# Kernel tuning notes

Hardware: AMD Instinct MI355X
Metric: run time of the kernel (lower is better)

## Reference

```python
import jax, jax.numpy as jnp
import numpy as np

H = 7      # n_hazards
B = 8      # batch
S = 2048   # seq_len
D = 768    # hidden_dim
K = 64     # bottleneck_dim
THR = 0.05 # influence_threshold


def setup_inputs() -> dict:
    key = jax.random.key(0)
    k0, k1, k2, k3 = jax.random.split(key, 4)
    x = jax.random.normal(k0, (H, B, S, D), jnp.float32)          # stacked hazard reprs
    M = jax.random.normal(k1, (H, H), jnp.float32) * 0.3           # interaction_matrix [src, tgt]
    W1 = jax.random.normal(k2, (H, H, D, K), jnp.float32) * (1.0 / np.sqrt(D).astype(np.float32))
    b1 = jnp.zeros((H, H, K), jnp.float32)
    W2 = jax.random.normal(k3, (H, H, K, D), jnp.float32) * (1.0 / np.sqrt(K).astype(np.float32))
    b2 = jnp.zeros((H, H, D), jnp.float32)
    return {"x": x, "M": M, "W1": W1, "b1": b1, "W2": W2, "b2": b2}


def reference(x, M, W1, b1, W2, b2):
    # Gate: influence used only if |M[s,t]| > threshold and s != t (torch skips the
    # projection entirely below threshold; masking to 0 yields identical values/grads).
    eye = jnp.eye(H, dtype=bool)
    gate = jnp.where((jnp.abs(M) > THR) & (~eye), M, jnp.zeros_like(M))  # [s, t]

    # Bottleneck MLP for all (source, target) pairs in one batched GEMM.
    # h: [s, t, b, n, k]
    h = jnp.einsum('sbnd,stdk->stbnk', x, W1) + b1[:, :, None, None, :]
    h = jax.nn.gelu(h, approximate=False)  # torch nn.GELU default is exact (erf)

    # Fold the scalar gate into the second GEMM so the [s,t,b,n,D] tensor is never
    # materialized; sum over sources lands directly at each target.
    add = jnp.einsum('st,stbnk,stkd->tbnd', gate, h, W2)
    add = add + jnp.einsum('st,std->td', gate, b2)[:, None, None, :]
    return x + add  # [H, B, S, D] stacked in hazard order
```

## Files before the change

kernel.cpp:

```cpp
#include <hip/hip_runtime.h>
#include <hip/hip_bf16.h>
#include <math.h>

#define NH   7
#define NROW 16384
#define DD   768
#define KK   64
#define THRG 0.05f

typedef float  f32x4   __attribute__((ext_vector_type(4)));
typedef __bf16 bf16x8  __attribute__((ext_vector_type(8)));
typedef short  short8v __attribute__((ext_vector_type(8)));
typedef short  short4v __attribute__((ext_vector_type(4)));

union V8 { short8v s; bf16x8 b; };

__device__ __forceinline__ float gate_of(const float* __restrict__ M, int s, int t) {
  float m = M[s * NH + t];
  return (s != t && fabsf(m) > THRG) ? m : 0.0f;
}

__device__ __forceinline__ float gelu_t(float v) {
  float u = 0.7978845608028654f * (v + 0.044715f * v * v * v);
  return v / (1.0f + __expf(-2.0f * u));
}

__device__ __forceinline__ void gload_lds16(const void* g, void* l) {
  __builtin_amdgcn_global_load_lds(
      (const __attribute__((address_space(1))) unsigned int*)g,
      (__attribute__((address_space(3))) unsigned int*)l, 16, 0, 0);
}

__global__ void prep_w1(const float* __restrict__ W1, unsigned short* __restrict__ W1P) {
  int pr = blockIdx.x;
  const float* src = W1 + (size_t)pr * DD * KK;
  __bf16* dst = (__bf16*)(W1P + (size_t)pr * 12 * 4096);
  for (int idx = threadIdx.x; idx < 12 * 4096; idx += blockDim.x) {
    int kc = idx >> 12, rem = idx & 4095;
    int kcol = rem >> 6, dl = rem & 63;
    int dl_log = dl ^ ((kcol & 7) << 3);
    dst[idx] = (__bf16)src[(size_t)(kc * 64 + dl_log) * KK + kcol];
  }
}

__global__ void prep_w2(const float* __restrict__ M, const float* __restrict__ W2,
                        unsigned short* __restrict__ W2P) {
  int st = blockIdx.x;
  int s = st / NH, t = st % NH;
  float g = gate_of(M, s, t);
  const float* src = W2 + (size_t)st * KK * DD;
  __bf16* dst = (__bf16*)(W2P + (size_t)((t * NH + s) * 6) * 8192);
  for (int idx = threadIdx.x; idx < 6 * 128 * 64; idx += blockDim.x) {
    int nb = idx >> 13, rem = idx & 8191;
    int dloc = rem >> 6, k = rem & 63;
    dst[idx] = (__bf16)(g * src[(size_t)k * DD + nb * 128 + dloc]);
  }
}

__global__ void prep_b2(const float* __restrict__ M, const float* __restrict__ b2,
                        float* __restrict__ b2sum) {
  int idx = blockIdx.x * blockDim.x + threadIdx.x;
  if (idx >= NH * DD) return;
  int t = idx / DD, d = idx % DD;
  float acc = 0.f;
  for (int s = 0; s < NH; ++s)
    acc += gate_of(M, s, t) * b2[(size_t)(s * NH + t) * DD + d];
  b2sum[idx] = acc;
}

__global__ __launch_bounds__(256, 3)
void chiA(const float* __restrict__ x, const float* __restrict__ M,
          const unsigned short* __restrict__ W1P, const float* __restrict__ b1,
          unsigned short* __restrict__ H) {
  __shared__ __align__(16) unsigned short xs[128 * 64];
  __shared__ __align__(16) unsigned short w1s[64 * 64];

  int bid = (int)blockIdx.x;
  int nid = (bid & 7) * 784 + (bid >> 3);
  int rb = nid / 49, pr = nid % 49;
  int s = pr / NH, t = pr % NH;
  if (gate_of(M, s, t) == 0.0f) return;
  int row0 = rb * 128;

  int tid = (int)threadIdx.x;
  int wid = tid >> 6, lane = tid & 63, l16 = lane & 15, l4 = lane >> 4;

  const f32x4 zero = {0.f, 0.f, 0.f, 0.f};
  f32x4 acc[4][2];
#pragma unroll
  for (int m = 0; m < 4; ++m)
#pragma unroll
    for (int n = 0; n < 2; ++n) acc[m][n] = zero;

  const float* xb = x + ((size_t)s * NROW + row0) * DD;
  const char* w1b = (const char*)(W1P + (size_t)pr * 12 * 4096);

  for (int kc = 0; kc < 12; ++kc) {
    __syncthreads();
    {
      const char* wsrc = w1b + (size_t)kc * 8192;
      char* wdst = (char*)w1s + (wid << 10);
#pragma unroll
      for (int r = 0; r < 2; ++r)
        gload_lds16(wsrc + r * 4096 + tid * 16, wdst + r * 4096);
    }
#pragma unroll
    for (int r = 0; r < 4; ++r) {
      int L = r * 4096 + tid * 16;
      int row = L >> 7, colB = L & 127;
      const float* gp = xb + (size_t)row * DD + kc * 64 + (colB >> 1);
      f32x4 v0 = *(const f32x4*)gp;
      f32x4 v1 = *(const f32x4*)(gp + 4);
      bf16x8 sv;
      sv[0] = (__bf16)v0[0]; sv[1] = (__bf16)v0[1];
      sv[2] = (__bf16)v0[2]; sv[3] = (__bf16)v0[3];
      sv[4] = (__bf16)v1[0]; sv[5] = (__bf16)v1[1];
      sv[6] = (__bf16)v1[2]; sv[7] = (__bf16)v1[3];
      *(bf16x8*)((char*)xs + (L ^ ((row & 7) << 4))) = sv;
    }
    __syncthreads();

    V8 af[4][2], bf2[2][2];
#pragma unroll
    for (int mm = 0; mm < 4; ++mm)
#pragma unroll
      for (int k2 = 0; k2 < 2; ++k2) {
        int rowl = mm * 16 + l16;
        int byte = (rowl * 128 + k2 * 64 + l4 * 16) ^ ((rowl & 7) << 4);
        af[mm][k2].s = *(const short8v*)((const char*)w1s + byte);
      }
#pragma unroll
    for (int nn = 0; nn < 2; ++nn)
#pragma unroll
      for (int k2 = 0; k2 < 2; ++k2) {
        int xr = wid * 32 + nn * 16 + l16;
        int byte = (xr * 128 + k2 * 64 + l4 * 16) ^ ((xr & 7) << 4);
        bf2[nn][k2].s = *(const short8v*)((const char*)xs + byte);
      }
#pragma unroll
    for (int k2 = 0; k2 < 2; ++k2)
#pragma unroll
      for (int mm = 0; mm < 4; ++mm)
#pragma unroll
        for (int nn = 0; nn < 2; ++nn)
          acc[mm][nn] = __builtin_amdgcn_mfma_f32_16x16x32_bf16(af[mm][k2].b, bf2[nn][k2].b, acc[mm][nn], 0, 0, 0);
  }

#pragma unroll
  for (int mm = 0; mm < 4; ++mm) {
    f32x4 bv = *(const f32x4*)(b1 + (size_t)pr * KK + mm * 16 + l4 * 4);
#pragma unroll
    for (int nn = 0; nn < 2; ++nn) {
      union { short4v s4; __bf16 b4[4]; } o;
#pragma unroll
      for (int r = 0; r < 4; ++r) o.b4[r] = (__bf16)gelu_t(acc[mm][nn][r] + bv[r]);
      int xrow = row0 + wid * 32 + nn * 16 + l16;
      unsigned short* hp = H + ((size_t)pr * NROW + xrow) * KK + mm * 16 + l4 * 4;
      *(short4v*)hp = o.s4;
    }
  }
}

__global__ __launch_bounds__(256, 4)
void chiB(const unsigned short* __restrict__ H, const float* __restrict__ x,
          const float* __restrict__ M, const unsigned short* __restrict__ W2P,
          const float* __restrict__ b2sum, float* __restrict__ out) {
  __shared__ __align__(16) unsigned short hs[128 * 64];
  __shared__ __align__(16) unsigned short w2s[128 * 64];

  int bid = (int)blockIdx.x;
  int nid = (bid & 7) * 672 + (bid >> 3);
  int nb = nid % 6, rem = nid / 6;
  int rb = rem % 128, t = rem / 128;
  int row0 = rb * 128, col0 = nb * 128;

  int tid = (int)threadIdx.x;
  int wid = tid >> 6, lane = tid & 63, l16 = lane & 15, l4 = lane >> 4;
  int wr = wid & 1, wc = wid >> 1;

  const f32x4 zero = {0.f, 0.f, 0.f, 0.f};
  f32x4 acc[4][4];
#pragma unroll
  for (int m = 0; m < 4; ++m)
#pragma unroll
    for (int n = 0; n < 4; ++n) acc[m][n] = zero;

  for (int s = 0; s < NH; ++s) {
    if (gate_of(M, s, t) == 0.0f) continue;
    __syncthreads();
    const char* hb = (const char*)(H + ((size_t)(s * NH + t) * NROW + row0) * KK);
    const char* wb = (const char*)(W2P + (size_t)((t * NH + s) * 6 + nb) * 8192);
#pragma unroll
    for (int r = 0; r < 4; ++r) {
      int L = r * 4096 + tid * 16;
      int row = L >> 7;
      short8v v = *(const short8v*)(hb + L);
      *(short8v*)((char*)hs + (L ^ ((row & 7) << 4))) = v;
      short8v w = *(const short8v*)(wb + L);
      *(short8v*)((char*)w2s + (L ^ ((row & 7) << 4))) = w;
    }
    __syncthreads();

    V8 af[4][2], bfr[4][2];
#pragma unroll
    for (int m = 0; m < 4; ++m)
#pragma unroll
      for (int k2 = 0; k2 < 2; ++k2) {
        int dl = wc * 64 + m * 16 + l16;
        int byte = (dl * 128 + k2 * 64 + l4 * 16) ^ ((dl & 7) << 4);
        af[m][k2].s = *(const short8v*)((const char*)w2s + byte);
      }
#pragma unroll
    for (int n = 0; n < 4; ++n)
#pragma unroll
      for (int k2 = 0; k2 < 2; ++k2) {
        int rl = wr * 64 + n * 16 + l16;
        int byte = (rl * 128 + k2 * 64 + l4 * 16) ^ ((rl & 7) << 4);
        bfr[n][k2].s = *(const short8v*)((const char*)hs + byte);
      }
#pragma unroll
    for (int k2 = 0; k2 < 2; ++k2)
#pragma unroll
      for (int m = 0; m < 4; ++m)
#pragma unroll
        for (int n = 0; n < 4; ++n)
          acc[m][n] = __builtin_amdgcn_mfma_f32_16x16x32_bf16(af[m][k2].b, bfr[n][k2].b, acc[m][n], 0, 0, 0);
  }

#pragma unroll
  for (int m = 0; m < 4; ++m) {
    int col = col0 + wc * 64 + m * 16 + l4 * 4;
    f32x4 bv = *(const f32x4*)(b2sum + (size_t)t * DD + col);
#pragma unroll
    for (int n = 0; n < 4; ++n) {
      int row = row0 + wr * 64 + n * 16 + l16;
      size_t off = ((size_t)t * NROW + row) * DD + col;
      f32x4 xv = *(const f32x4*)(x + off);
      f32x4 ov;
#pragma unroll
      for (int r = 0; r < 4; ++r) ov[r] = acc[m][n][r] + xv[r] + bv[r];
      *(f32x4*)(out + off) = ov;
    }
  }
}

extern "C" void kernel_launch(void* const* d_in, const int* in_sizes, int n_in,
                              void* d_out, int out_size, void* d_ws, size_t ws_size,
                              hipStream_t stream) {
  const float* x  = (const float*)d_in[0];
  const float* M  = (const float*)d_in[1];
  const float* W1 = (const float*)d_in[2];
  const float* b1 = (const float*)d_in[3];
  const float* W2 = (const float*)d_in[4];
  const float* b2 = (const float*)d_in[5];
  float* out = (float*)d_out;

  char* ws = (char*)d_ws;
  unsigned short* W1P = (unsigned short*)ws;
  unsigned short* W2P = (unsigned short*)(ws + 4816896);
  float* b2sum        = (float*)(ws + 9633792);
  unsigned short* H   = (unsigned short*)(ws + 9655296);

  prep_w1<<<dim3(49), dim3(256), 0, stream>>>(W1, W1P);
  prep_w2<<<dim3(49), dim3(256), 0, stream>>>(M, W2, W2P);
  prep_b2<<<dim3((NH * DD + 255) / 256), dim3(256), 0, stream>>>(M, b2, b2sum);
  chiA<<<dim3(128 * 49), dim3(256), 0, stream>>>(x, M, W1P, b1, H);
  chiB<<<dim3(NH * 128 * 6), dim3(256), 0, stream>>>(H, x, M, W2P, b2sum, out);
}
```

Measured before the change: 485.8 us.

## Software-pipeline chiA K-loop with register prefetch of x and double-buffered W1

Restructures the first-GEMM K loop so the next chunk's x tile is loaded into registers and the next W1 tile is staged asynchronously into a second LDS buffer while the current chunk runs MFMAs. The goal is to hide global-load latency behind compute instead of serialising load, sync and compute. In exchange it raises register pressure by holding eight prefetched float4 vectors, doubles the W1 LDS footprint, and adds one extra barrier per iteration, which may reduce occupancy under the launch bound of three blocks.

Result: slower. 525.3 us (+8.1%).

```diff
diff --git a/kernel.cpp b/kernel.cpp
--- a/kernel.cpp
+++ b/kernel.cpp
@@ -73,7 +73,7 @@
           const unsigned short* __restrict__ W1P, const float* __restrict__ b1,
           unsigned short* __restrict__ H) {
   __shared__ __align__(16) unsigned short xs[128 * 64];
-  __shared__ __align__(16) unsigned short w1s[64 * 64];
+  __shared__ __align__(16) unsigned short w1s[2][64 * 64];
 
   int bid = (int)blockIdx.x;
   int nid = (bid & 7) * 784 + (bid >> 3);
@@ -95,31 +95,42 @@
   const float* xb = x + ((size_t)s * NROW + row0) * DD;
   const char* w1b = (const char*)(W1P + (size_t)pr * 12 * 4096);
 
-  for (int kc = 0; kc < 12; ++kc) {
-    __syncthreads();
-    {
-      const char* wsrc = w1b + (size_t)kc * 8192;
-      char* wdst = (char*)w1s + (wid << 10);
-#pragma unroll
-      for (int r = 0; r < 2; ++r)
-        gload_lds16(wsrc + r * 4096 + tid * 16, wdst + r * 4096);
-    }
+  f32x4 xr[8];
+
+  auto LOADX = [&](int kc) {
 #pragma unroll
     for (int r = 0; r < 4; ++r) {
       int L = r * 4096 + tid * 16;
       int row = L >> 7, colB = L & 127;
       const float* gp = xb + (size_t)row * DD + kc * 64 + (colB >> 1);
-      f32x4 v0 = *(const f32x4*)gp;
-      f32x4 v1 = *(const f32x4*)(gp + 4);
+      xr[2 * r]     = *(const f32x4*)gp;
+      xr[2 * r + 1] = *(const f32x4*)(gp + 4);
+    }
+  };
+
+  auto STAGEW1 = [&](int kc, int p) {
+    const char* wsrc = w1b + (size_t)kc * 8192;
+    char* wdst = (char*)w1s[p] + (wid << 10);
+#pragma unroll
+    for (int r = 0; r < 2; ++r)
+      gload_lds16(wsrc + r * 4096 + tid * 16, wdst + r * 4096);
+  };
+
+  auto CVTWRITE = [&]() {
+#pragma unroll
+    for (int r = 0; r < 4; ++r) {
+      int L = r * 4096 + tid * 16;
+      int row = L >> 7;
       bf16x8 sv;
-      sv[0] = (__bf16)v0[0]; sv[1] = (__bf16)v0[1];
-      sv[2] = (__bf16)v0[2]; sv[3] = (__bf16)v0[3];
-      sv[4] = (__bf16)v1[0]; sv[5] = (__bf16)v1[1];
-      sv[6] = (__bf16)v1[2]; sv[7] = (__bf16)v1[3];
+      sv[0] = (__bf16)xr[2*r][0]; sv[1] = (__bf16)xr[2*r][1];
+      sv[2] = (__bf16)xr[2*r][2]; sv[3] = (__bf16)xr[2*r][3];
+      sv[4] = (__bf16)xr[2*r+1][0]; sv[5] = (__bf16)xr[2*r+1][1];
+      sv[6] = (__bf16)xr[2*r+1][2]; sv[7] = (__bf16)xr[2*r+1][3];
       *(bf16x8*)((char*)xs + (L ^ ((row & 7) << 4))) = sv;
     }
-    __syncthreads();
-
+  };
+
+  auto COMPUTE = [&](int p) {
     V8 af[4][2], bf2[2][2];
 #pragma unroll
     for (int mm = 0; mm < 4; ++mm)
@@ -127,14 +138,14 @@
       for (int k2 = 0; k2 < 2; ++k2) {
         int rowl = mm * 16 + l16;
         int byte = (rowl * 128 + k2 * 64 + l4 * 16) ^ ((rowl & 7) << 4);
-        af[mm][k2].s = *(const short8v*)((const char*)w1s + byte);
+        af[mm][k2].s = *(const short8v*)((const char*)w1s[p] + byte);
       }
 #pragma unroll
     for (int nn = 0; nn < 2; ++nn)
 #pragma unroll
       for (int k2 = 0; k2 < 2; ++k2) {
-        int xr = wid * 32 + nn * 16 + l16;
-        int byte = (xr * 128 + k2 * 64 + l4 * 16) ^ ((xr & 7) << 4);
+        int xrw = wid * 32 + nn * 16 + l16;
+        int byte = (xrw * 128 + k2 * 64 + l4 * 16) ^ ((xrw & 7) << 4);
         bf2[nn][k2].s = *(const short8v*)((const char*)xs + byte);
       }
 #pragma unroll
@@ -144,6 +155,20 @@
 #pragma unroll
         for (int nn = 0; nn < 2; ++nn)
           acc[mm][nn] = __builtin_amdgcn_mfma_f32_16x16x32_bf16(af[mm][k2].b, bf2[nn][k2].b, acc[mm][nn], 0, 0, 0);
+  };
+
+  LOADX(0);
+  STAGEW1(0, 0);
+  CVTWRITE();
+  __syncthreads();
+  int p = 0;
+  for (int kc = 0; kc < 12; ++kc) {
+    if (kc < 11) { LOADX(kc + 1); STAGEW1(kc + 1, p ^ 1); }
+    COMPUTE(p);
+    __syncthreads();
+    if (kc < 11) CVTWRITE();
+    __syncthreads();
+    p ^= 1;
   }
 
 #pragma unroll
```

## Compute two target hazards per chiA block to reuse the loaded x tile

Applied to the files above, without the earlier changes.

Each chiA block now handles one source hazard and a pair of targets, so each x tile is loaded and converted to bf16 once and used for two W1 projections instead of one. The grid shrinks from 6272 to 3584 blocks, and the launch-bounds occupancy hint is dropped. The goal is to roughly halve the fp32 x reads from global memory and the conversion work in the first GEMM stage. In exchange each block holds two accumulator sets and a second W1 LDS buffer, which raises register and LDS pressure, and the 7th target slot is often empty, which wastes part of a block.

Result: faster. 446.0 us (-8.2%).

```diff
diff --git a/kernel.cpp b/kernel.cpp
--- a/kernel.cpp
+++ b/kernel.cpp
@@ -68,38 +68,52 @@
   b2sum[idx] = acc;
 }
 
-__global__ __launch_bounds__(256, 3)
+__global__ __launch_bounds__(256)
 void chiA(const float* __restrict__ x, const float* __restrict__ M,
           const unsigned short* __restrict__ W1P, const float* __restrict__ b1,
           unsigned short* __restrict__ H) {
   __shared__ __align__(16) unsigned short xs[128 * 64];
-  __shared__ __align__(16) unsigned short w1s[64 * 64];
+  __shared__ __align__(16) unsigned short w1s0[64 * 64];
+  __shared__ __align__(16) unsigned short w1s1[64 * 64];
 
   int bid = (int)blockIdx.x;
-  int nid = (bid & 7) * 784 + (bid >> 3);
-  int rb = nid / 49, pr = nid % 49;
-  int s = pr / NH, t = pr % NH;
-  if (gate_of(M, s, t) == 0.0f) return;
+  int nid = (bid & 7) * 448 + (bid >> 3);
+  int tg = nid & 3;  int rem = nid >> 2;
+  int s = rem % NH, rb = rem / NH;
+  int t0 = tg * 2, t1 = tg * 2 + 1;
+  float g0 = gate_of(M, s, t0);
+  float g1 = (t1 < NH) ? gate_of(M, s, t1) : 0.0f;
+  bool a0 = (g0 != 0.0f), a1 = (g1 != 0.0f);
+  if (!a0 && !a1) return;
+  int pr0 = s * NH + t0, pr1 = s * NH + t1;
   int row0 = rb * 128;
 
   int tid = (int)threadIdx.x;
   int wid = tid >> 6, lane = tid & 63, l16 = lane & 15, l4 = lane >> 4;
 
   const f32x4 zero = {0.f, 0.f, 0.f, 0.f};
-  f32x4 acc[4][2];
+  f32x4 acc0[4][2], acc1[4][2];
 #pragma unroll
   for (int m = 0; m < 4; ++m)
 #pragma unroll
-    for (int n = 0; n < 2; ++n) acc[m][n] = zero;
+    for (int n = 0; n < 2; ++n) { acc0[m][n] = zero; acc1[m][n] = zero; }
 
   const float* xb = x + ((size_t)s * NROW + row0) * DD;
-  const char* w1b = (const char*)(W1P + (size_t)pr * 12 * 4096);
+  const char* w1b0 = (const char*)(W1P + (size_t)pr0 * 12 * 4096);
+  const char* w1b1 = (const char*)(W1P + (size_t)pr1 * 12 * 4096);
 
   for (int kc = 0; kc < 12; ++kc) {
     __syncthreads();
-    {
-      const char* wsrc = w1b + (size_t)kc * 8192;
-      char* wdst = (char*)w1s + (wid << 10);
+    if (a0) {
+      const char* wsrc = w1b0 + (size_t)kc * 8192;
+      char* wdst = (char*)w1s0 + (wid << 10);
+#pragma unroll
+      for (int r = 0; r < 2; ++r)
+        gload_lds16(wsrc + r * 4096 + tid * 16, wdst + r * 4096);
+    }
+    if (a1) {
+      const char* wsrc = w1b1 + (size_t)kc * 8192;
+      char* wdst = (char*)w1s1 + (wid << 10);
 #pragma unroll
       for (int r = 0; r < 2; ++r)
         gload_lds16(wsrc + r * 4096 + tid * 16, wdst + r * 4096);
@@ -120,15 +134,7 @@
     }
     __syncthreads();
 
-    V8 af[4][2], bf2[2][2];
-#pragma unroll
-    for (int mm = 0; mm < 4; ++mm)
-#pragma unroll
-      for (int k2 = 0; k2 < 2; ++k2) {
-        int rowl = mm * 16 + l16;
-        int byte = (rowl * 128 + k2 * 64 + l4 * 16) ^ ((rowl & 7) << 4);
-        af[mm][k2].s = *(const short8v*)((const char*)w1s + byte);
-      }
+    V8 bf2[2][2];
 #pragma unroll
     for (int nn = 0; nn < 2; ++nn)
 #pragma unroll
@@ -137,26 +143,72 @@
         int byte = (xr * 128 + k2 * 64 + l4 * 16) ^ ((xr & 7) << 4);
         bf2[nn][k2].s = *(const short8v*)((const char*)xs + byte);
       }
-#pragma unroll
-    for (int k2 = 0; k2 < 2; ++k2)
+    if (a0) {
+      V8 af[4][2];
 #pragma unroll
       for (int mm = 0; mm < 4; ++mm)
 #pragma unroll
-        for (int nn = 0; nn < 2; ++nn)
-          acc[mm][nn] = __builtin_amdgcn_mfma_f32_16x16x32_bf16(af[mm][k2].b, bf2[nn][k2].b, acc[mm][nn], 0, 0, 0);
-  }
-
-#pragma unroll
-  for (int mm = 0; mm < 4; ++mm) {
-    f32x4 bv = *(const f32x4*)(b1 + (size_t)pr * KK + mm * 16 + l4 * 4);
-#pragma unroll
-    for (int nn = 0; nn < 2; ++nn) {
-      union { short4v s4; __bf16 b4[4]; } o;
-#pragma unroll
-      for (int r = 0; r < 4; ++r) o.b4[r] = (__bf16)gelu_t(acc[mm][nn][r] + bv[r]);
-      int xrow = row0 + wid * 32 + nn * 16 + l16;
-      unsigned short* hp = H + ((size_t)pr * NROW + xrow) * KK + mm * 16 + l4 * 4;
-      *(short4v*)hp = o.s4;
+        for (int k2 = 0; k2 < 2; ++k2) {
+          int rowl = mm * 16 + l16;
+          int byte = (rowl * 128 + k2 * 64 + l4 * 16) ^ ((rowl & 7) << 4);
+          af[mm][k2].s = *(const short8v*)((const char*)w1s0 + byte);
+        }
+#pragma unroll
+      for (int k2 = 0; k2 < 2; ++k2)
+#pragma unroll
+        for (int mm = 0; mm < 4; ++mm)
+#pragma unroll
+          for (int nn = 0; nn < 2; ++nn)
+            acc0[mm][nn] = __builtin_amdgcn_mfma_f32_16x16x32_bf16(af[mm][k2].b, bf2[nn][k2].b, acc0[mm][nn], 0, 0, 0);
+    }
+    if (a1) {
+      V8 af[4][2];
+#pragma unroll
+      for (int mm = 0; mm < 4; ++mm)
+#pragma unroll
+        for (int k2 = 0; k2 < 2; ++k2) {
+          int rowl = mm * 16 + l16;
+          int byte = (rowl * 128 + k2 * 64 + l4 * 16) ^ ((rowl & 7) << 4);
+          af[mm][k2].s = *(const short8v*)((const char*)w1s1 + byte);
+        }
+#pragma unroll
+      for (int k2 = 0; k2 < 2; ++k2)
+#pragma unroll
+        for (int mm = 0; mm < 4; ++mm)
+#pragma unroll
+          for (int nn = 0; nn < 2; ++nn)
+            acc1[mm][nn] = __builtin_amdgcn_mfma_f32_16x16x32_bf16(af[mm][k2].b, bf2[nn][k2].b, acc1[mm][nn], 0, 0, 0);
+    }
+  }
+
+  if (a0) {
+#pragma unroll
+    for (int mm = 0; mm < 4; ++mm) {
+      f32x4 bv = *(const f32x4*)(b1 + (size_t)pr0 * KK + mm * 16 + l4 * 4);
+#pragma unroll
+      for (int nn = 0; nn < 2; ++nn) {
+        union { short4v s4; __bf16 b4[4]; } o;
+#pragma unroll
+        for (int r = 0; r < 4; ++r) o.b4[r] = (__bf16)gelu_t(acc0[mm][nn][r] + bv[r]);
+        int xrow = row0 + wid * 32 + nn * 16 + l16;
+        unsigned short* hp = H + ((size_t)pr0 * NROW + xrow) * KK + mm * 16 + l4 * 4;
+        *(short4v*)hp = o.s4;
+      }
+    }
+  }
+  if (a1) {
+#pragma unroll
+    for (int mm = 0; mm < 4; ++mm) {
+      f32x4 bv = *(const f32x4*)(b1 + (size_t)pr1 * KK + mm * 16 + l4 * 4);
+#pragma unroll
+      for (int nn = 0; nn < 2; ++nn) {
+        union { short4v s4; __bf16 b4[4]; } o;
+#pragma unroll
+        for (int r = 0; r < 4; ++r) o.b4[r] = (__bf16)gelu_t(acc1[mm][nn][r] + bv[r]);
+        int xrow = row0 + wid * 32 + nn * 16 + l16;
+        unsigned short* hp = H + ((size_t)pr1 * NROW + xrow) * KK + mm * 16 + l4 * 4;
+        *(short4v*)hp = o.s4;
+      }
     }
   }
 }
@@ -264,6 +316,6 @@
   prep_w1<<<dim3(49), dim3(256), 0, stream>>>(W1, W1P);
   prep_w2<<<dim3(49), dim3(256), 0, stream>>>(M, W2, W2P);
   prep_b2<<<dim3((NH * DD + 255) / 256), dim3(256), 0, stream>>>(M, b2, b2sum);
-  chiA<<<dim3(128 * 49), dim3(256), 0, stream>>>(x, M, W1P, b1, H);
+  chiA<<<dim3(3584), dim3(256), 0, stream>>>(x, M, W1P, b1, H);
   chiB<<<dim3(NH * 128 * 6), dim3(256), 0, stream>>>(H, x, M, W2P, b2sum, out);
 }
```
